# Optimization experiments

Measured on AMD Instinct MI355X. Metric: run time of the kernel, lower is better.

Reference implementation:

```python
import jax, jax.numpy as jnp
import numpy as np

IN_CH = 512
NUM_HEADS = 8
DEPTH = IN_CH // NUM_HEADS
IN_FEAT = 37


def setup_inputs() -> dict:
    key = jax.random.key(0)
    ks = jax.random.split(key, 9)
    B, S = 4, 2048
    s_in = 1.0 / np.sqrt(IN_FEAT)
    s_ch = 1.0 / np.sqrt(IN_CH)
    return {
        "x": jax.random.normal(ks[0], (B, S, IN_FEAT), dtype=jnp.float32),
        "Wq": jax.random.uniform(ks[1], (IN_FEAT, IN_CH), jnp.float32, -s_in, s_in),
        "bq": jax.random.uniform(ks[2], (IN_CH,), jnp.float32, -s_in, s_in),
        "Wk": jax.random.uniform(ks[3], (IN_FEAT, IN_CH), jnp.float32, -s_in, s_in),
        "bk": jax.random.uniform(ks[4], (IN_CH,), jnp.float32, -s_in, s_in),
        "Wv": jax.random.uniform(ks[5], (IN_FEAT, IN_CH), jnp.float32, -s_in, s_in),
        "bv": jax.random.uniform(ks[6], (IN_CH,), jnp.float32, -s_in, s_in),
        "Wd": jax.random.uniform(ks[7], (IN_CH, IN_CH), jnp.float32, -s_ch, s_ch),
        "bd": jax.random.uniform(ks[8], (IN_CH,), jnp.float32, -s_ch, s_ch),
    }


def reference(x, Wq, bq, Wk, bk, Wv, bv, Wd, bd):
    B, S, _ = x.shape
    # projections: [B,S,in_ch] -> split into [B,S,H,D]
    q = (x @ Wq + bq).reshape(B, S, NUM_HEADS, DEPTH)
    k = (x @ Wk + bk).reshape(B, S, NUM_HEADS, DEPTH)
    v = (x @ Wv + bv).reshape(B, S, NUM_HEADS, DEPTH)
    scale = 1.0 / jnp.sqrt(jnp.float32(DEPTH))
    # scores: [B,H,Sq,Sk]
    logits = jnp.einsum("bqhd,bkhd->bhqk", q, k) * scale
    attn = jax.nn.softmax(logits, axis=-1)
    out = jnp.einsum("bhqk,bkhd->bqhd", attn, v).reshape(B, S, IN_CH)
    return out @ Wd + bd
```

## Files before the change

### kernel.cpp

```cpp
#include <hip/hip_runtime.h>
#include <hip/hip_bf16.h>
#include <stdint.h>

#define IN_FEAT 37
#define IN_CH 512
#define NUM_HEADS 8
#define DEPTH 64
#define BB 4
#define SS 2048
#define NROWS (BB * SS)

typedef unsigned short u16;
typedef __attribute__((ext_vector_type(8))) short bf16x8;
typedef __attribute__((ext_vector_type(4))) float f32x4;
typedef __attribute__((ext_vector_type(16))) float f32x16;
typedef __attribute__((ext_vector_type(4))) unsigned u32x4;

#define MFMA16(a, b, c) __builtin_amdgcn_mfma_f32_16x16x32_bf16(a, b, c, 0, 0, 0)
#define MFMA32(a, b, c) __builtin_amdgcn_mfma_f32_32x32x16_bf16(a, b, c, 0, 0, 0)

#define GLDS16(gsrc, ldst)                                                          \
    __builtin_amdgcn_global_load_lds(                                               \
        reinterpret_cast<const __attribute__((address_space(1))) void*>(            \
            reinterpret_cast<uintptr_t>(gsrc)),                                     \
        reinterpret_cast<__attribute__((address_space(3))) void*>(                  \
            reinterpret_cast<uintptr_t>(ldst)),                                     \
        16, 0, 0)

__device__ __forceinline__ u16 f2bf(float f) {
    union { float f; unsigned u; } v;
    v.f = f;
    unsigned r = v.u + 0x7fffu + ((v.u >> 16) & 1u);
    return (u16)(r >> 16);
}

__device__ __forceinline__ unsigned cvt_pk_bf16(float a, float b) {
    unsigned r;
    asm("v_cvt_pk_bf16_f32 %0, %1, %2" : "=v"(r) : "v"(a), "v"(b));
    return r;
}

#define XB_ELEMS (NROWS * 64)
#define WT_ELEMS (IN_CH * 64)
#define WD_ELEMS (IN_CH * IN_CH)
#define PACK_TOTAL (XB_ELEMS + 3 * WT_ELEMS + WD_ELEMS)

__global__ __launch_bounds__(256) void pack_all(
    const float* __restrict__ x,
    const float* __restrict__ Wq, const float* __restrict__ Wk,
    const float* __restrict__ Wv, const float* __restrict__ Wd,
    u16* __restrict__ xb, u16* __restrict__ WqT, u16* __restrict__ WkT,
    u16* __restrict__ WvT, u16* __restrict__ WdT)
{
    const float QSC = 0.125f * 1.44269504f;
    int idx = blockIdx.x * 256 + threadIdx.x;
    if (idx < XB_ELEMS) {
        int row = idx >> 6, col = idx & 63;
        xb[idx] = (col < IN_FEAT) ? f2bf(x[row * IN_FEAT + col]) : (u16)0;
    } else if (idx < XB_ELEMS + 3 * WT_ELEMS) {
        int j = idx - XB_ELEMS;
        int mat = j >> 15, rem = j & (WT_ELEMS - 1);
        int c = rem >> 6, i = rem & 63;
        float v = 0.f;
        if (i < IN_FEAT) {
            if (mat == 0)      v = Wq[i * IN_CH + c] * QSC;
            else if (mat == 1) v = Wk[i * IN_CH + c];
            else               v = Wv[i * IN_CH + c];
        }
        (mat == 0 ? WqT : mat == 1 ? WkT : WvT)[rem] = f2bf(v);
    } else if (idx < PACK_TOTAL) {
        int j = idx - (XB_ELEMS + 3 * WT_ELEMS);
        int r = j >> 9, c = j & 511;
        WdT[c * IN_CH + r] = f2bf(Wd[j]);
    }
}

__global__ __launch_bounds__(256) void proj_qk(
    const u16* __restrict__ xb, const u16* __restrict__ WqT,
    const u16* __restrict__ WkT, const float* __restrict__ bqp,
    const float* __restrict__ bkp, u16* __restrict__ qo, u16* __restrict__ ko)
{
    const float QSC = 0.125f * 1.44269504f;
    const int tid = threadIdx.x;
    const int w = tid >> 6, lane = tid & 63;
    const int g = lane >> 4, l15 = lane & 15;
    const int m0 = blockIdx.x * 64 + w * 16;
    const int n0 = blockIdx.y * 64;
    const f32x4 Z4 = {0.f, 0.f, 0.f, 0.f};

    f32x4 aq[4], ak[4];
#pragma unroll
    for (int nt = 0; nt < 4; ++nt) { aq[nt] = Z4; ak[nt] = Z4; }

#pragma unroll
    for (int k0 = 0; k0 < 64; k0 += 32) {
        bf16x8 a = *(const bf16x8*)&xb[(m0 + l15) * 64 + k0 + g * 8];
#pragma unroll
        for (int nt = 0; nt < 4; ++nt) {
            bf16x8 bq8 = *(const bf16x8*)&WqT[(n0 + nt * 16 + l15) * 64 + k0 + g * 8];
            bf16x8 bk8 = *(const bf16x8*)&WkT[(n0 + nt * 16 + l15) * 64 + k0 + g * 8];
            aq[nt] = MFMA16(a, bq8, aq[nt]);
            ak[nt] = MFMA16(a, bk8, ak[nt]);
        }
    }
#pragma unroll
    for (int nt = 0; nt < 4; ++nt) {
        const int n = n0 + nt * 16 + l15;
        const float bqv = bqp[n] * QSC, bkv = bkp[n];
        const int h = n >> 6, d = n & 63;
#pragma unroll
        for (int r = 0; r < 4; ++r) {
            const int m = m0 + g * 4 + r;
            const int b = m >> 11, s = m & 2047;
            const int bh = b * NUM_HEADS + h;
            qo[(bh * SS + s) * DEPTH + d] = f2bf(aq[nt][r] + bqv);
            ko[bh * (SS * 64) + (s >> 6) * 4096 + (s & 63) * 64 + (d ^ ((s & 7) << 3))] =
                f2bf(ak[nt][r] + bkv);
        }
    }
}

__global__ __launch_bounds__(256) void proj_vT(
    const u16* __restrict__ WvT, const u16* __restrict__ xb,
    const float* __restrict__ bvp, u16* __restrict__ vo)
{
    const int tid = threadIdx.x;
    const int w = tid >> 6, lane = tid & 63;
    const int g = lane >> 4, l15 = lane & 15;
    const int m0 = blockIdx.x * 64 + w * 16;
    const int n0 = blockIdx.y * 64;
    const f32x4 Z4 = {0.f, 0.f, 0.f, 0.f};

    f32x4 acc[4];
#pragma unroll
    for (int nt = 0; nt < 4; ++nt) acc[nt] = Z4;

#pragma unroll
    for (int k0 = 0; k0 < 64; k0 += 32) {
        bf16x8 a = *(const bf16x8*)&WvT[(m0 + l15) * 64 + k0 + g * 8];
#pragma unroll
        for (int nt = 0; nt < 4; ++nt) {
            bf16x8 b8 = *(const bf16x8*)&xb[(n0 + nt * 16 + l15) * 64 + k0 + g * 8];
            acc[nt] = MFMA16(a, b8, acc[nt]);
        }
    }
    float bvr[4];
#pragma unroll
    for (int r = 0; r < 4; ++r) bvr[r] = bvp[m0 + g * 4 + r];
#pragma unroll
    for (int nt = 0; nt < 4; ++nt) {
#pragma unroll
        for (int r = 0; r < 4; ++r) {
            const int c = m0 + g * 4 + r;
            const int rr = n0 + nt * 16 + l15;
            const int b = rr >> 11, s = rr & 2047;
            const int h = c >> 6, d = c & 63;
            const int bh = b * NUM_HEADS + h;
            vo[bh * (SS * 64) + (s >> 6) * 4096 + d * 64 + ((s & 63) ^ ((d & 7) << 3))] =
                f2bf(acc[nt][r] + bvr[r]);
        }
    }
}

#define NT (SS / 64)

__global__ __launch_bounds__(256) void attn_kernel(
    const u16* __restrict__ Qm, const u16* __restrict__ Km,
    const u16* __restrict__ Vm, u16* __restrict__ Om)
{
    __shared__ u16 KL[4][2][2048];
    const int tid = threadIdx.x;
    const int w = tid >> 6, lane = tid & 63;
    const int r31 = lane & 31, lh = lane >> 5;
    const int qgrp = w >> 1, kh = w & 1;

    const int lin = blockIdx.x + gridDim.x * blockIdx.y;
    const int xcd = lin & 7, t7 = lin >> 3;
    const int bx = t7 & 31, bh = xcd + 8 * (t7 >> 5);
    const int qbase = bx * 64 + qgrp * 32;

    const u16* ktg = Km + bh * (SS * 64) + kh * 2048;
    const u16* vtg = Vm + bh * (SS * 64);

    bf16x8 Qf[4];
#pragma unroll
    for (int c = 0; c < 4; ++c)
        Qf[c] = *(const bf16x8*)&Qm[(bh * SS + qbase + r31) * 64 + c * 16 + lh * 8];

    f32x16 O0, O1;
#pragma unroll
    for (int i = 0; i < 16; ++i) { O0[i] = 0.f; O1[i] = 0.f; }
    float lreg = 0.f;

    auto STAGE_K = [&](int buf, int t) {
        const u16* ks = ktg + t * 4096 + lane * 8;
        u16* kd = &KL[w][buf][0];
#pragma unroll
        for (int i = 0; i < 4; ++i) GLDS16(ks + i * 512, kd + i * 512);
    };
    auto VLOAD = [&](bf16x8 (&v)[4], int t) {
        const u16* vt = vtg + t * 4096;
#pragma unroll
        for (int dt = 0; dt < 2; ++dt)
#pragma unroll
            for (int o = 0; o < 2; ++o) {
                const int vrow = dt * 32 + r31;
                v[dt * 2 + o] = *(const bf16x8*)
                    &vt[vrow * 64 + ((kh * 32 + o * 16 + lh * 8) ^ ((vrow & 7) << 3))];
            }
    };

    auto STEP = [&](int buf, bf16x8 (&v)[4], int t, int waitN, bool stage) {
        if (waitN == 8) asm volatile("s_waitcnt vmcnt(8)" ::: "memory");
        else            asm volatile("s_waitcnt vmcnt(0)" ::: "memory");
        __builtin_amdgcn_sched_barrier(0);

        const u16* kb = &KL[w][buf][0];
        bf16x8 kf[4];
#pragma unroll
        for (int c = 0; c < 4; ++c)
            kf[c] = *(const bf16x8*)&kb[r31 * 64 + ((c * 16 + lh * 8) ^ ((r31 & 7) << 3))];

        f32x16 s;
#pragma unroll
        for (int i = 0; i < 16; ++i) s[i] = 0.f;
#pragma unroll
        for (int c = 0; c < 4; ++c) s = MFMA32(kf[c], Qf[c], s);

        unsigned pk[8];
        float ps = 0.f;
#pragma unroll
        for (int j = 0; j < 8; ++j) {
            float a = exp2f(s[2 * j]);
            float b = exp2f(s[2 * j + 1]);
            ps += a + b;
            pk[j] = cvt_pk_bf16(a, b);
        }
        lreg += ps;

        asm("v_permlane32_swap_b32 %0, %1" : "+v"(pk[0]), "+v"(pk[2]));
        asm("v_permlane32_swap_b32 %0, %1" : "+v"(pk[1]), "+v"(pk[3]));
        asm("v_permlane32_swap_b32 %0, %1" : "+v"(pk[4]), "+v"(pk[6]));
        asm("v_permlane32_swap_b32 %0, %1" : "+v"(pk[5]), "+v"(pk[7]));

        union { u32x4 u; bf16x8 b; } f0, f1;
        f0.u = (u32x4){pk[0], pk[1], pk[2], pk[3]};
        f1.u = (u32x4){pk[4], pk[5], pk[6], pk[7]};

        if (stage) {
            asm volatile("s_waitcnt lgkmcnt(0)" ::: "memory");
            __builtin_amdgcn_sched_barrier(0);
            STAGE_K(buf, t + 2);
        }

        O0 = MFMA32(f0.b, v[0], O0);
        O0 = MFMA32(f1.b, v[1], O0);
        O1 = MFMA32(f0.b, v[2], O1);
        O1 = MFMA32(f1.b, v[3], O1);

        if (stage) VLOAD(v, t + 2);
    };

    bf16x8 vA[4], vB[4];
    STAGE_K(0, 0);
    VLOAD(vA, 0);
    STAGE_K(1, 1);
    VLOAD(vB, 1);

    for (int tt = 0; tt < NT - 2; tt += 2) {
        STEP(0, vA, tt,     8, tt + 2 < NT);
        STEP(1, vB, tt + 1, 8, tt + 3 < NT);
    }
    STEP(0, vA, NT - 2, 8, false);
    STEP(1, vB, NT - 1, 0, false);

    asm volatile("s_waitcnt vmcnt(0)" ::: "memory");
    __syncthreads();
    float lfull = lreg + __shfl_xor(lreg, 32, 64);
    float* sc = (float*)&KL[0][0][0];
    float* scp = sc + qgrp * 2112;
    if (kh == 1) {
#pragma unroll
        for (int i = 0; i < 16; ++i) scp[i * 64 + lane] = O0[i];
#pragma unroll
        for (int i = 0; i < 16; ++i) scp[(16 + i) * 64 + lane] = O1[i];
        scp[2048 + lane] = lfull;
    }
    __syncthreads();
    if (kh == 0) {
#pragma unroll
        for (int i = 0; i < 16; ++i) O0[i] += scp[i * 64 + lane];
#pragma unroll
        for (int i = 0; i < 16; ++i) O1[i] += scp[(16 + i) * 64 + lane];
        const float inv = 1.0f / (lfull + scp[2048 + lane]);
        const int b = bh >> 3, hh = bh & 7;
#pragma unroll
        for (int i = 0; i < 16; ++i) {
            const int qr = (i & 3) + 8 * (i >> 2) + 4 * lh;
            const float invq = __shfl(inv, qr, 64);
            const int srow = qbase + qr;
            u16* orow = &Om[((b * SS + srow) << 9) + hh * 64];
            orow[r31]      = f2bf(O0[i] * invq);
            orow[32 + r31] = f2bf(O1[i] * invq);
        }
    }
}

__global__ __launch_bounds__(256) void out_gemm(
    const u16* __restrict__ A, const u16* __restrict__ BT,
    const float* __restrict__ bd, float* __restrict__ out)
{
    const int tid = threadIdx.x;
    const int w = tid >> 6, lane = tid & 63;
    const int g = lane >> 4, l15 = lane & 15;
    const int m0 = blockIdx.x * 64 + w * 16;
    const int n0 = blockIdx.y * 64;
    const f32x4 Z4 = {0.f, 0.f, 0.f, 0.f};

    f32x4 acc[4];
#pragma unroll
    for (int nt = 0; nt < 4; ++nt) acc[nt] = Z4;

    for (int k0 = 0; k0 < IN_CH; k0 += 32) {
        bf16x8 a = *(const bf16x8*)&A[(m0 + l15) * IN_CH + k0 + g * 8];
#pragma unroll
        for (int nt = 0; nt < 4; ++nt) {
            bf16x8 b = *(const bf16x8*)&BT[(n0 + nt * 16 + l15) * IN_CH + k0 + g * 8];
            acc[nt] = MFMA16(a, b, acc[nt]);
        }
    }
#pragma unroll
    for (int nt = 0; nt < 4; ++nt)
#pragma unroll
        for (int r = 0; r < 4; ++r) {
            const int m = m0 + g * 4 + r;
            const int n = n0 + nt * 16 + l15;
            out[m * IN_CH + n] = acc[nt][r] + bd[n];
        }
}

extern "C" void kernel_launch(void* const* d_in, const int* in_sizes, int n_in,
                              void* d_out, int out_size, void* d_ws, size_t ws_size,
                              hipStream_t stream)
{
    const float* x  = (const float*)d_in[0];
    const float* Wq = (const float*)d_in[1];
    const float* bq = (const float*)d_in[2];
    const float* Wk = (const float*)d_in[3];
    const float* bk = (const float*)d_in[4];
    const float* Wv = (const float*)d_in[5];
    const float* bv = (const float*)d_in[6];
    const float* Wd = (const float*)d_in[7];
    const float* bd = (const float*)d_in[8];
    float* out = (float*)d_out;

    u16* ws  = (u16*)d_ws;
    u16* q   = ws;
    u16* k   = q + NROWS * IN_CH;
    u16* vT  = k + NROWS * IN_CH;
    u16* ao  = vT + NROWS * IN_CH;
    u16* WdT = ao + NROWS * IN_CH;
    u16* xb  = WdT + WD_ELEMS;
    u16* WqT = xb + XB_ELEMS;
    u16* WkT = WqT + WT_ELEMS;
    u16* WvT = WkT + WT_ELEMS;

    pack_all<<<dim3((PACK_TOTAL + 255) / 256), dim3(256), 0, stream>>>(
        x, Wq, Wk, Wv, Wd, xb, WqT, WkT, WvT, WdT);
    proj_qk<<<dim3(NROWS / 64, IN_CH / 64), dim3(256), 0, stream>>>(
        xb, WqT, WkT, bq, bk, q, k);
    proj_vT<<<dim3(IN_CH / 64, NROWS / 64), dim3(256), 0, stream>>>(
        WvT, xb, bv, vT);
    attn_kernel<<<dim3(SS / 64, BB * NUM_HEADS), dim3(256), 0, stream>>>(q, k, vT, ao);
    out_gemm<<<dim3(NROWS / 64, IN_CH / 64), dim3(256), 0, stream>>>(ao, WdT, bd, out);
}
```

Before: 136.5 us.

## Drop V register double-buffering, raise occupancy hint, use raw v_exp_f32

Replaces the unrolled two-step loop, which prefetched V fragments into registers two tiles ahead, with a simple per-tile loop. That loop loads V directly at the top of each iteration and issues the next K LDS stage right after the QK MFMAs. It adds a launch-bounds hint for 4 blocks per SM and swaps exp2f for an inline v_exp_f32 to skip the library wrapper. The intent is to cut register pressure so more waves can run, and to start K staging earlier. The risk is that V global-load latency is now only hidden by the QK MFMAs and exp work within the same iteration.

```diff
diff --git a/kernel.cpp b/kernel.cpp
--- a/kernel.cpp
+++ b/kernel.cpp
@@ -37,6 +37,12 @@
 __device__ __forceinline__ unsigned cvt_pk_bf16(float a, float b) {
     unsigned r;
     asm("v_cvt_pk_bf16_f32 %0, %1, %2" : "=v"(r) : "v"(a), "v"(b));
+    return r;
+}
+
+__device__ __forceinline__ float fexp2(float x) {
+    float r;
+    asm("v_exp_f32 %0, %1" : "=v"(r) : "v"(x));
     return r;
 }
 
@@ -164,7 +170,7 @@
 
 #define NT (SS / 64)
 
-__global__ __launch_bounds__(256) void attn_kernel(
+__global__ __launch_bounds__(256, 4) void attn_kernel(
     const u16* __restrict__ Qm, const u16* __restrict__ Km,
     const u16* __restrict__ Vm, u16* __restrict__ Om)
 {
@@ -187,9 +193,9 @@
     for (int c = 0; c < 4; ++c)
         Qf[c] = *(const bf16x8*)&Qm[(bh * SS + qbase + r31) * 64 + c * 16 + lh * 8];
 
-    f32x16 O0, O1;
-#pragma unroll
-    for (int i = 0; i < 16; ++i) { O0[i] = 0.f; O1[i] = 0.f; }
+    f32x16 O0, O1, Z16;
+#pragma unroll
+    for (int i = 0; i < 16; ++i) { O0[i] = 0.f; O1[i] = 0.f; Z16[i] = 0.f; }
     float lreg = 0.f;
 
     auto STAGE_K = [&](int buf, int t) {
@@ -198,41 +204,51 @@
 #pragma unroll
         for (int i = 0; i < 4; ++i) GLDS16(ks + i * 512, kd + i * 512);
     };
-    auto VLOAD = [&](bf16x8 (&v)[4], int t) {
-        const u16* vt = vtg + t * 4096;
-#pragma unroll
-        for (int dt = 0; dt < 2; ++dt)
-#pragma unroll
-            for (int o = 0; o < 2; ++o) {
-                const int vrow = dt * 32 + r31;
-                v[dt * 2 + o] = *(const bf16x8*)
-                    &vt[vrow * 64 + ((kh * 32 + o * 16 + lh * 8) ^ ((vrow & 7) << 3))];
-            }
-    };
-
-    auto STEP = [&](int buf, bf16x8 (&v)[4], int t, int waitN, bool stage) {
-        if (waitN == 8) asm volatile("s_waitcnt vmcnt(8)" ::: "memory");
+
+    STAGE_K(0, 0);
+    STAGE_K(1, 1);
+
+    for (int t = 0; t < NT; ++t) {
+        if (t < NT - 1) asm volatile("s_waitcnt vmcnt(4)" ::: "memory");
         else            asm volatile("s_waitcnt vmcnt(0)" ::: "memory");
         __builtin_amdgcn_sched_barrier(0);
 
-        const u16* kb = &KL[w][buf][0];
+        bf16x8 v[4];
+        {
+            const u16* vt = vtg + t * 4096;
+#pragma unroll
+            for (int dt = 0; dt < 2; ++dt)
+#pragma unroll
+                for (int o = 0; o < 2; ++o) {
+                    const int vrow = dt * 32 + r31;
+                    v[dt * 2 + o] = *(const bf16x8*)
+                        &vt[vrow * 64 + ((kh * 32 + o * 16 + lh * 8) ^ ((vrow & 7) << 3))];
+                }
+        }
+
+        const u16* kb = &KL[w][t & 1][0];
         bf16x8 kf[4];
 #pragma unroll
         for (int c = 0; c < 4; ++c)
             kf[c] = *(const bf16x8*)&kb[r31 * 64 + ((c * 16 + lh * 8) ^ ((r31 & 7) << 3))];
 
-        f32x16 s;
-#pragma unroll
-        for (int i = 0; i < 16; ++i) s[i] = 0.f;
-#pragma unroll
-        for (int c = 0; c < 4; ++c) s = MFMA32(kf[c], Qf[c], s);
+        f32x16 s = MFMA32(kf[0], Qf[0], Z16);
+        s = MFMA32(kf[1], Qf[1], s);
+        s = MFMA32(kf[2], Qf[2], s);
+        s = MFMA32(kf[3], Qf[3], s);
+
+        if (t + 2 < NT) {
+            asm volatile("s_waitcnt lgkmcnt(0)" ::: "memory");
+            __builtin_amdgcn_sched_barrier(0);
+            STAGE_K(t & 1, t + 2);
+        }
 
         unsigned pk[8];
         float ps = 0.f;
 #pragma unroll
         for (int j = 0; j < 8; ++j) {
-            float a = exp2f(s[2 * j]);
-            float b = exp2f(s[2 * j + 1]);
+            float a = fexp2(s[2 * j]);
+            float b = fexp2(s[2 * j + 1]);
             ps += a + b;
             pk[j] = cvt_pk_bf16(a, b);
         }
@@ -247,32 +263,11 @@
         f0.u = (u32x4){pk[0], pk[1], pk[2], pk[3]};
         f1.u = (u32x4){pk[4], pk[5], pk[6], pk[7]};
 
-        if (stage) {
-            asm volatile("s_waitcnt lgkmcnt(0)" ::: "memory");
-            __builtin_amdgcn_sched_barrier(0);
-            STAGE_K(buf, t + 2);
-        }
-
         O0 = MFMA32(f0.b, v[0], O0);
         O0 = MFMA32(f1.b, v[1], O0);
         O1 = MFMA32(f0.b, v[2], O1);
         O1 = MFMA32(f1.b, v[3], O1);
-
-        if (stage) VLOAD(v, t + 2);
-    };
-
-    bf16x8 vA[4], vB[4];
-    STAGE_K(0, 0);
-    VLOAD(vA, 0);
-    STAGE_K(1, 1);
-    VLOAD(vB, 1);
-
-    for (int tt = 0; tt < NT - 2; tt += 2) {
-        STEP(0, vA, tt,     8, tt + 2 < NT);
-        STEP(1, vB, tt + 1, 8, tt + 3 < NT);
-    }
-    STEP(0, vA, NT - 2, 8, false);
-    STEP(1, vB, NT - 1, 0, false);
+    }
 
     asm volatile("s_waitcnt vmcnt(0)" ::: "memory");
     __syncthreads();
```

Result: faster. 123.8 us (-9.3%).
